# Optimization experiments

Measured on AMD Instinct MI355X. Metric: run time of the kernel, lower is better.

## Reference

```python
import jax, jax.numpy as jnp
import numpy as np

B_, T_, D_ = 8, 4096, 1024  # batch, seq_len, input_dim == state_dim


def setup_inputs() -> dict:
    key = jax.random.key(0)
    ks = jax.random.split(key, 9)
    s = 1.0 / np.sqrt(D_)  # nn.Linear default init scale
    return {
        "u":   jax.random.normal(ks[0], (B_, T_, D_), dtype=jnp.float32),
        "WA":  jax.random.uniform(ks[1], (D_, D_), jnp.float32, -s, s),
        "WB":  jax.random.uniform(ks[2], (D_, D_), jnp.float32, -s, s),
        "WAf": jax.random.uniform(ks[3], (D_, D_), jnp.float32, -s, s),
        "WBf": jax.random.uniform(ks[4], (D_, D_), jnp.float32, -s, s),
        "w1":  jax.random.uniform(ks[5], (1, D_), jnp.float32, -s, s),
        "w2":  jax.random.uniform(ks[6], (1, D_), jnp.float32, -s, s),
        "b":   jnp.zeros((1,), dtype=jnp.float32),
        "Wc":  jax.random.uniform(ks[7], (1, D_), jnp.float32, -s, s),
    }


def reference(u, WA, WB, WAf, WBf, w1, w2, b, Wc):
    # NOTE: the torch loop reads x_forward/x_backward from the pre-loop zeros
    # tensor, so A(.)/Af(.) are always applied to zeros. Actual math:
    #   x_f[0] = u[0];      x_f[t]   = B  u[t]    for t >= 1
    #   x_b[T-1] = u[T-1];  x_b[t]   = Bf u[t+1]  for t <= T-2
    bsz, seq_len, _ = u.shape
    xf = jnp.concatenate([u[:, :1], jnp.einsum('btd,ed->bte', u[:, 1:], WB)], axis=1)
    xb = jnp.concatenate([jnp.einsum('btd,ed->bte', u[:, 1:], WBf), u[:, -1:]], axis=1)
    gamma = jax.nn.sigmoid(xf @ w1.T + xb @ w2.T + b)       # (b, t, 1)
    y = gamma * (xf + xb) + (1.0 - gamma) * u               # (b, t, d)
    final_output = jax.nn.sigmoid(y @ Wc.T).reshape(bsz, seq_len)
    return y, gamma, final_output
```

## Files before the change

kernel.cpp:

```cpp
#include <hip/hip_runtime.h>
#include <hip/hip_bf16.h>
#include <cstddef>

#define GLOBAL_AS __attribute__((address_space(1)))
#define LDS_AS __attribute__((address_space(3)))

typedef __bf16 bf16_t;
typedef __bf16 bf16x8 __attribute__((ext_vector_type(8)));
typedef __bf16 bf16x4 __attribute__((ext_vector_type(4)));
typedef float f32x4 __attribute__((ext_vector_type(4)));

static constexpr int Tseq  = 4096;
static constexpr int Dd    = 1024;
static constexpr int Mrows = 8 * 4096;
static constexpr int UGRP  = 8388608;

__global__ __launch_bounds__(256) void k_prep(const float* __restrict__ u,
                                              const float* __restrict__ WB,
                                              const float* __restrict__ WBf,
                                              bf16_t* __restrict__ u16,
                                              bf16_t* __restrict__ wcat) {
    const int i = blockIdx.x * 256 + threadIdx.x;
    if (i < UGRP) {
        float4 v = reinterpret_cast<const float4*>(u)[i];
        bf16x4 o;
        o[0] = (__bf16)v.x; o[1] = (__bf16)v.y; o[2] = (__bf16)v.z; o[3] = (__bf16)v.w;
        reinterpret_cast<bf16x4*>(u16)[i] = o;
    } else {
        const int j  = i - UGRP;
        const int e4 = j * 4;
        const float* s = (e4 < 1024 * 1024) ? (WB + e4) : (WBf + (e4 - 1024 * 1024));
        float4 v = *reinterpret_cast<const float4*>(s);
        bf16x4 o;
        o[0] = (__bf16)v.x; o[1] = (__bf16)v.y; o[2] = (__bf16)v.z; o[3] = (__bf16)v.w;
        reinterpret_cast<bf16x4*>(wcat)[j] = o;
    }
}

__global__ __launch_bounds__(512, 2) void k_gemm(const bf16_t* __restrict__ A,
                                                 const bf16_t* __restrict__ Bt,
                                                 bf16_t* __restrict__ xf,
                                                 bf16_t* __restrict__ xb) {
    __shared__ __align__(16) char sm[131072];

    const int tid  = threadIdx.x;
    const int wid  = tid >> 6;
    const int lane = tid & 63;
    const int lane15 = lane & 15;
    const int g16  = (lane >> 4) * 16;
    const int wmq  = wid >> 1;
    const int wnq  = wid & 1;

    const int bid0 = blockIdx.x;
    const int swzb = (bid0 & 7) * 128 + (bid0 >> 3);
    const int bcol = swzb & 7;
    const int brow = swzb >> 3;

    const int srow = tid >> 3;
    const int scol = ((tid & 7) ^ (srow & 7)) * 8;
    const bf16_t* gA = A  + ((size_t)brow * 256 + srow) * 1024 + scol;
    const bf16_t* gB = Bt + ((size_t)bcol * 256 + srow) * 1024 + scol;

    char* const smw = sm + wid * 1024;

    f32x4 acc[2][2][2][4] = {};
    bf16x8 afr[2][2][2];
    bf16x8 bfr[4][2];

#define STAGE(bufb, isA, h, kt1) do {                                          \
    const bf16_t* _s = ((isA) ? gA : gB) + (size_t)(h) * 131072 + (kt1) * 64;  \
    char* _l = smw + (bufb) * 65536 + ((isA) ? 0 : 32768) + (h) * 16384;       \
    __builtin_amdgcn_global_load_lds((const GLOBAL_AS void*)_s,                \
                                     (LDS_AS void*)_l, 16, 0, 0);              \
    __builtin_amdgcn_global_load_lds((const GLOBAL_AS void*)(_s + 65536),      \
                                     (LDS_AS void*)(_l + 8192), 16, 0, 0);     \
} while (0)

#define RD_A(bufb, mhh) do {                                                   \
    _Pragma("unroll") for (int mi = 0; mi < 2; ++mi) {                         \
      const int rr = wmq * 32 + mi * 16 + lane15;                              \
      const char* _p = sm + (bufb) * 65536 + (mhh) * 16384 + rr * 128;         \
      const int sz = (rr & 7) << 4;                                            \
      _Pragma("unroll") for (int kk = 0; kk < 2; ++kk)                         \
        afr[mhh][mi][kk] = *reinterpret_cast<const bf16x8*>(_p + ((kk * 64 + g16) ^ sz)); \
    } } while (0)

#define RD_B(bufb, nhh) do {                                                   \
    _Pragma("unroll") for (int ni = 0; ni < 4; ++ni) {                         \
      const int rr = wnq * 64 + ni * 16 + lane15;                              \
      const char* _p = sm + (bufb) * 65536 + 32768 + (nhh) * 16384 + rr * 128; \
      const int sz = (rr & 7) << 4;                                            \
      _Pragma("unroll") for (int kk = 0; kk < 2; ++kk)                         \
        bfr[ni][kk] = *reinterpret_cast<const bf16x8*>(_p + ((kk * 64 + g16) ^ sz)); \
    } } while (0)

#define MM(MH, NH) do {                                                        \
    __builtin_amdgcn_s_setprio(1);                                             \
    _Pragma("unroll") for (int kk = 0; kk < 2; ++kk)                           \
    _Pragma("unroll") for (int mi = 0; mi < 2; ++mi)                           \
    _Pragma("unroll") for (int ni = 0; ni < 4; ++ni)                           \
      acc[MH][mi][NH][ni] = __builtin_amdgcn_mfma_f32_16x16x32_bf16(           \
          afr[MH][mi][kk], bfr[ni][kk], acc[MH][mi][NH][ni], 0, 0, 0);         \
    __builtin_amdgcn_s_setprio(0);                                             \
} while (0)

#define BARM() asm volatile("s_barrier" ::: "memory")

    STAGE(0, 1, 0, 0);
    STAGE(0, 0, 0, 0);
    STAGE(0, 1, 1, 0);
    STAGE(0, 0, 1, 0);
    asm volatile("s_waitcnt vmcnt(4)" ::: "memory");
    BARM();

#pragma unroll 2
    for (int t = 0; t < 16; ++t) {
        const int buf = t & 1;
        const bool pf = t < 15;
        const int k1 = t + 1;
        RD_A(buf, 0); RD_B(buf, 0);
        if (pf) STAGE(buf ^ 1, 1, 0, k1);
        __builtin_amdgcn_s_barrier();
        MM(0, 0);
        if (pf) { asm volatile("s_waitcnt vmcnt(4)" ::: "memory"); }
        else    { asm volatile("s_waitcnt vmcnt(2)" ::: "memory"); }
        BARM();
        RD_A(buf, 1);
        if (pf) STAGE(buf ^ 1, 0, 0, k1);
        __builtin_amdgcn_s_barrier();
        MM(1, 0);
        if (pf) { asm volatile("s_waitcnt vmcnt(4)" ::: "memory"); }
        else    { asm volatile("s_waitcnt vmcnt(0)" ::: "memory"); }
        BARM();
        RD_B(buf, 1);
        if (pf) STAGE(buf ^ 1, 1, 1, k1);
        __builtin_amdgcn_s_barrier();
        MM(1, 1);
        BARM();
        if (pf) STAGE(buf ^ 1, 0, 1, k1);
        __builtin_amdgcn_s_barrier();
        MM(0, 1);
        if (pf) { asm volatile("s_waitcnt vmcnt(4)" ::: "memory"); }
        BARM();
    }

    const bool isF  = bcol < 4;
    const int rbase = brow * 256 + wmq * 32 + (lane >> 4) * 4;
    const int cb0   = bcol * 256 + wnq * 64 + lane15;
    #pragma unroll
    for (int mh = 0; mh < 2; ++mh)
    #pragma unroll
    for (int mi = 0; mi < 2; ++mi)
    #pragma unroll
    for (int j = 0; j < 4; ++j) {
        const int r = rbase + mh * 128 + mi * 16 + j;
        #pragma unroll
        for (int nh = 0; nh < 2; ++nh)
        #pragma unroll
        for (int ni = 0; ni < 4; ++ni) {
            const int c = cb0 + nh * 128 + ni * 16;
            const __bf16 v = (__bf16)acc[mh][mi][nh][ni][j];
            if (isF)         xf[(size_t)r * 1024 + c] = v;
            else if (r >= 1) xb[(size_t)(r - 1) * 1024 + (c - 1024)] = v;
        }
    }
#undef STAGE
#undef RD_A
#undef RD_B
#undef MM
#undef BARM
}

__global__ __launch_bounds__(256) void k_epi(const bf16_t* __restrict__ u16,
                                             const bf16_t* __restrict__ xf,
                                             const bf16_t* __restrict__ xb,
                                             const float* __restrict__ w1,
                                             const float* __restrict__ w2,
                                             const float* __restrict__ bb,
                                             const float* __restrict__ Wc,
                                             float* __restrict__ y,
                                             float* __restrict__ gout,
                                             float* __restrict__ fout) {
    const int lane = threadIdx.x & 63;
    const int r0   = blockIdx.x * 8 + (threadIdx.x >> 6) * 2;

    bf16x8 u8[2][2], f8[2][2], b8[2][2];
    #pragma unroll
    for (int rr = 0; rr < 2; ++rr) {
        const size_t rb = (size_t)(r0 + rr) * Dd;
        #pragma unroll
        for (int j = 0; j < 2; ++j) {
            const int e = j * 512 + lane * 8;
            u8[rr][j] = *reinterpret_cast<const bf16x8*>(u16 + rb + e);
            f8[rr][j] = *reinterpret_cast<const bf16x8*>(xf + rb + e);
            b8[rr][j] = *reinterpret_cast<const bf16x8*>(xb + rb + e);
        }
    }
    float w1v[16], w2v[16], wcv[16];
    #pragma unroll
    for (int j = 0; j < 2; ++j) {
        const int e = j * 512 + lane * 8;
        #pragma unroll
        for (int i = 0; i < 8; ++i) {
            w1v[j*8+i] = w1[e + i];
            w2v[j*8+i] = w2[e + i];
            wcv[j*8+i] = Wc[e + i];
        }
    }

    float uv[2][16], xfv[2][16], xbv[2][16];
    #pragma unroll
    for (int rr = 0; rr < 2; ++rr) {
        const int t = (r0 + rr) & (Tseq - 1);
        #pragma unroll
        for (int j = 0; j < 2; ++j) {
            #pragma unroll
            for (int i = 0; i < 8; ++i) {
                uv[rr][j*8+i]  = (float)u8[rr][j][i];
                xfv[rr][j*8+i] = (float)f8[rr][j][i];
                xbv[rr][j*8+i] = (float)b8[rr][j][i];
            }
        }
        if (t == 0) {
            #pragma unroll
            for (int i = 0; i < 16; ++i) xfv[rr][i] = uv[rr][i];
        }
        if (t == Tseq - 1) {
            #pragma unroll
            for (int i = 0; i < 16; ++i) xbv[rr][i] = uv[rr][i];
        }
    }

    float part[2] = {0.0f, 0.0f};
    #pragma unroll
    for (int rr = 0; rr < 2; ++rr)
        #pragma unroll
        for (int i = 0; i < 16; ++i)
            part[rr] += xfv[rr][i] * w1v[i] + xbv[rr][i] * w2v[i];
    #pragma unroll
    for (int off = 32; off >= 1; off >>= 1) {
        part[0] += __shfl_xor(part[0], off);
        part[1] += __shfl_xor(part[1], off);
    }
    const float bias = bb[0];
    float g[2];
    g[0] = 1.0f / (1.0f + __expf(-(part[0] + bias)));
    g[1] = 1.0f / (1.0f + __expf(-(part[1] + bias)));

    float p2[2] = {0.0f, 0.0f};
    #pragma unroll
    for (int rr = 0; rr < 2; ++rr) {
        const size_t rb = (size_t)(r0 + rr) * Dd;
        #pragma unroll
        for (int j = 0; j < 4; ++j) {
            float4 yv;
            const int e = (j >> 1) * 512 + lane * 8 + (j & 1) * 4;
            const int q = (j >> 1) * 8 + (j & 1) * 4;
            yv.x = g[rr] * (xfv[rr][q+0] + xbv[rr][q+0]) + (1.0f - g[rr]) * uv[rr][q+0];
            yv.y = g[rr] * (xfv[rr][q+1] + xbv[rr][q+1]) + (1.0f - g[rr]) * uv[rr][q+1];
            yv.z = g[rr] * (xfv[rr][q+2] + xbv[rr][q+2]) + (1.0f - g[rr]) * uv[rr][q+2];
            yv.w = g[rr] * (xfv[rr][q+3] + xbv[rr][q+3]) + (1.0f - g[rr]) * uv[rr][q+3];
            *reinterpret_cast<float4*>(y + rb + e) = yv;
            p2[rr] += yv.x * wcv[q+0] + yv.y * wcv[q+1] + yv.z * wcv[q+2] + yv.w * wcv[q+3];
        }
    }
    #pragma unroll
    for (int off = 32; off >= 1; off >>= 1) {
        p2[0] += __shfl_xor(p2[0], off);
        p2[1] += __shfl_xor(p2[1], off);
    }
    if (lane == 0) {
        gout[r0]     = g[0];
        gout[r0 + 1] = g[1];
        fout[r0]     = 1.0f / (1.0f + __expf(-p2[0]));
        fout[r0 + 1] = 1.0f / (1.0f + __expf(-p2[1]));
    }
}

extern "C" void kernel_launch(void* const* d_in, const int* in_sizes, int n_in,
                              void* d_out, int out_size, void* d_ws, size_t ws_size,
                              hipStream_t stream) {
    const float* u   = (const float*)d_in[0];
    const float* WB  = (const float*)d_in[2];
    const float* WBf = (const float*)d_in[4];
    const float* w1  = (const float*)d_in[5];
    const float* w2  = (const float*)d_in[6];
    const float* bb  = (const float*)d_in[7];
    const float* Wc  = (const float*)d_in[8];

    char* ws = (char*)d_ws;
    bf16_t* u16  = (bf16_t*)(ws);
    bf16_t* wcat = (bf16_t*)(ws + 67108864);
    bf16_t* xfw  = (bf16_t*)(ws + 71303168);
    bf16_t* xbw  = (bf16_t*)(ws + 138412032);

    float* y    = (float*)d_out;
    float* gout = y + (size_t)Mrows * Dd;
    float* fout = gout + Mrows;

    k_prep<<<dim3(34816), dim3(256), 0, stream>>>(u, WB, WBf, u16, wcat);

    k_gemm<<<dim3(1024), dim3(512), 0, stream>>>(u16, wcat, xfw, xbw);

    k_epi<<<dim3(Mrows / 8), dim3(256), 0, stream>>>(u16, xfw, xbw, w1, w2, bb, Wc,
                                                     y, gout, fout);
}
```

Measured before the change: 425.2 us.

## Merge GEMM main-loop phases to cut barriers and vectorize weight loads

The GEMM inner loop now has two phases per k-step instead of four. It reads both A halves up front and issues three prefetch stages together, so each barrier covers two MFMA blocks. The vmcnt thresholds are adjusted to match the new count of outstanding loads, and setprio now wraps the paired MFMA groups. Separately, the epilogue kernel loads w1, w2 and Wc as float4 instead of scalars. Fewer barriers should reduce synchronization stalls, at the cost of more live A fragments (register pressure) and less overlap between each prefetch and the compute that follows it.

```diff
diff --git a/kernel.cpp b/kernel.cpp
--- a/kernel.cpp
+++ b/kernel.cpp
@@ -95,13 +95,11 @@
     } } while (0)
 
 #define MM(MH, NH) do {                                                        \
-    __builtin_amdgcn_s_setprio(1);                                             \
     _Pragma("unroll") for (int kk = 0; kk < 2; ++kk)                           \
     _Pragma("unroll") for (int mi = 0; mi < 2; ++mi)                           \
     _Pragma("unroll") for (int ni = 0; ni < 4; ++ni)                           \
       acc[MH][mi][NH][ni] = __builtin_amdgcn_mfma_f32_16x16x32_bf16(           \
           afr[MH][mi][kk], bfr[ni][kk], acc[MH][mi][NH][ni], 0, 0, 0);         \
-    __builtin_amdgcn_s_setprio(0);                                             \
 } while (0)
 
 #define BARM() asm volatile("s_barrier" ::: "memory")
@@ -110,7 +108,7 @@
     STAGE(0, 0, 0, 0);
     STAGE(0, 1, 1, 0);
     STAGE(0, 0, 1, 0);
-    asm volatile("s_waitcnt vmcnt(4)" ::: "memory");
+    asm volatile("s_waitcnt vmcnt(2)" ::: "memory");
     BARM();
 
 #pragma unroll 2
@@ -118,29 +116,22 @@
         const int buf = t & 1;
         const bool pf = t < 15;
         const int k1 = t + 1;
-        RD_A(buf, 0); RD_B(buf, 0);
-        if (pf) STAGE(buf ^ 1, 1, 0, k1);
+        RD_A(buf, 0); RD_A(buf, 1); RD_B(buf, 0);
+        if (pf) { STAGE(buf ^ 1, 1, 0, k1); STAGE(buf ^ 1, 0, 0, k1); STAGE(buf ^ 1, 1, 1, k1); }
         __builtin_amdgcn_s_barrier();
-        MM(0, 0);
-        if (pf) { asm volatile("s_waitcnt vmcnt(4)" ::: "memory"); }
-        else    { asm volatile("s_waitcnt vmcnt(2)" ::: "memory"); }
-        BARM();
-        RD_A(buf, 1);
-        if (pf) STAGE(buf ^ 1, 0, 0, k1);
-        __builtin_amdgcn_s_barrier();
-        MM(1, 0);
-        if (pf) { asm volatile("s_waitcnt vmcnt(4)" ::: "memory"); }
+        __builtin_amdgcn_s_setprio(1);
+        MM(0, 0); MM(1, 0);
+        __builtin_amdgcn_s_setprio(0);
+        if (pf) { asm volatile("s_waitcnt vmcnt(6)" ::: "memory"); }
         else    { asm volatile("s_waitcnt vmcnt(0)" ::: "memory"); }
         BARM();
         RD_B(buf, 1);
-        if (pf) STAGE(buf ^ 1, 1, 1, k1);
-        __builtin_amdgcn_s_barrier();
-        MM(1, 1);
-        BARM();
         if (pf) STAGE(buf ^ 1, 0, 1, k1);
         __builtin_amdgcn_s_barrier();
-        MM(0, 1);
-        if (pf) { asm volatile("s_waitcnt vmcnt(4)" ::: "memory"); }
+        __builtin_amdgcn_s_setprio(1);
+        MM(1, 1); MM(0, 1);
+        __builtin_amdgcn_s_setprio(0);
+        if (pf) { asm volatile("s_waitcnt vmcnt(2)" ::: "memory"); }
         BARM();
     }
 
@@ -199,12 +190,16 @@
     float w1v[16], w2v[16], wcv[16];
     #pragma unroll
     for (int j = 0; j < 2; ++j) {
-        const int e = j * 512 + lane * 8;
-        #pragma unroll
-        for (int i = 0; i < 8; ++i) {
-            w1v[j*8+i] = w1[e + i];
-            w2v[j*8+i] = w2[e + i];
-            wcv[j*8+i] = Wc[e + i];
+        const int q4 = j * 128 + lane * 2;
+        #pragma unroll
+        for (int h = 0; h < 2; ++h) {
+            const float4 a = reinterpret_cast<const float4*>(w1)[q4 + h];
+            const float4 c = reinterpret_cast<const float4*>(w2)[q4 + h];
+            const float4 w = reinterpret_cast<const float4*>(Wc)[q4 + h];
+            const int o = j * 8 + h * 4;
+            w1v[o+0] = a.x; w1v[o+1] = a.y; w1v[o+2] = a.z; w1v[o+3] = a.w;
+            w2v[o+0] = c.x; w2v[o+1] = c.y; w2v[o+2] = c.z; w2v[o+3] = c.w;
+            wcv[o+0] = w.x; wcv[o+1] = w.y; wcv[o+2] = w.z; wcv[o+3] = w.w;
         }
     }
 
```

After: 429.6 us. No clear change (+1.0%).
